# Kernel tuning notes

Measured on AMD Instinct MI355X. Metric: run time of the kernel, lower is better.

## Reference

```python
import jax, jax.numpy as jnp
import numpy as np

S = 3      # num_scales
CIN = 3    # in_channels (hardcoded by expand(...,3,...) in source)
COUT = 3   # out_channels (forced by final broadcast)
K = 3
PAD = 1


def setup_inputs() -> dict:
    key = jax.random.key(0)
    ks = jax.random.split(key, 8)
    B, H, W = 4, 384, 384
    x = jax.random.normal(ks[0], (B, CIN, H, W), jnp.float32)
    # params follow the torch inits: theta,sigma ~ U(0,pi); f0,theta0 = 1
    theta = jax.random.uniform(ks[1], (S, COUT, CIN), jnp.float32) * jnp.pi
    sigma = jax.random.uniform(ks[2], (S, COUT, CIN), jnp.float32) * jnp.pi
    f0 = jnp.ones((S, COUT, CIN), jnp.float32)
    theta0 = jnp.ones((S, COUT, CIN), jnp.float32)
    attn_w1 = jax.random.normal(ks[3], (64, CIN), jnp.float32) * 0.1     # 1x1 conv weight
    attn_b1 = jnp.zeros((64,), jnp.float32)
    attn_w2 = jax.random.normal(ks[4], (COUT * S, 64), jnp.float32) * 0.1
    attn_b2 = jnp.zeros((COUT * S,), jnp.float32)
    conv_w = jax.random.normal(ks[5], (COUT, CIN, K, K), jnp.float32) * 0.05
    mixing = jax.random.uniform(ks[6], (1,), jnp.float32)
    band = jax.random.uniform(ks[7], (COUT, CIN, 2), jnp.float32)        # freq_band_select ~ U(0,1)
    return dict(x=x, theta=theta, sigma=sigma, f0=f0, theta0=theta0,
                attn_w1=attn_w1, attn_b1=attn_b1, attn_w2=attn_w2, attn_b2=attn_b2,
                conv_w=conv_w, mixing=mixing, band=band)


def _log_gabor_bank(theta, sigma, f0, theta0, H, W):
    # vectorized over all scales: returns [S, Co, Cin, H, W] real filter bank
    yy, xx = jnp.meshgrid(jnp.linspace(-1.0, 1.0, H), jnp.linspace(-1.0, 1.0, W), indexing='ij')
    r = jnp.sqrt(xx * xx + yy * yy + 1e-6)          # [H,W]
    phi = jnp.arctan2(yy, xx)                        # [H,W]
    f0e = f0[..., None, None]                        # [S,Co,Cin,1,1]
    sig = sigma[..., None, None]
    th = theta[..., None, None]
    th0 = theta0[..., None, None]
    log_gabor = jnp.exp(-jnp.log(r - jnp.log(f0e)) ** 2 / (2.0 * jnp.log(sig) ** 2))
    angular = jnp.exp(-(phi - th) ** 2 / (2.0 * th0 ** 2))
    return log_gabor * angular


def _forward(x, theta, sigma, f0, theta0, attn_w1, attn_b1, attn_w2, attn_b2, conv_w, mixing, band):
    B, Cin, H, W = x.shape
    # torch.fft.fftshift with no dim shifts ALL axes (incl. batch/channel) -- replicate exactly
    x_freq_shift = jnp.fft.fftshift(jnp.fft.fft2(x))                 # [B,Cin,H,W] complex64

    filt = _log_gabor_bank(theta, sigma, f0, theta0, H, W)           # [S,Co,Cin,H,W]

    # attention net: 1x1 conv -> relu -> 1x1 conv -> softmax over channel dim
    mag = jnp.abs(x_freq_shift)
    h1 = jax.nn.relu(jnp.einsum('bchw,oc->bohw', mag, attn_w1) + attn_b1[None, :, None, None])
    logits = jnp.einsum('bchw,oc->bohw', h1, attn_w2) + attn_b2[None, :, None, None]
    attn = jax.nn.softmax(logits, axis=1).reshape(B, S, COUT, H, W)

    # attended[b,d,h,w] = sum_{s,co} attn[b,s,co,h,w] * xfreq[b,d,h,w] * filt[s,co,d,h,w]
    wgt = jnp.einsum('bschw,scdhw->bdhw', attn, filt)                # real [B,Cin,H,W]
    attended = (x_freq_shift * wgt).sum(axis=1)                      # [B,H,W] complex

    # per-(out,in)-channel square band mask, indices from height (as in source)
    start_idx = jnp.floor((band[..., 0] + 1.0) / 2.0 * H).astype(jnp.int32)   # [Co,Cin]
    end_idx = jnp.floor((band[..., 1] + 1.0) / 2.0 * H).astype(jnp.int32)
    ih = jnp.arange(H)
    rm = (ih[None, None, :] >= start_idx[..., None]) & (ih[None, None, :] < end_idx[..., None])
    iw = jnp.arange(W)
    cm = (iw[None, None, :] >= start_idx[..., None]) & (iw[None, None, :] < end_idx[..., None])
    mask = (rm[..., :, None] & cm[..., None, :]).astype(x.dtype)     # [Co,Cin,H,W]

    # broadcast quirk in source: [B,1,H,W] * [B,Co,1,Cin,H,W] -> [B,Co,B,Cin,H,W]
    six = mask[None, :, None, :, :, :] * attended[None, None, :, None, :, :]
    six = jnp.broadcast_to(six, (B, COUT, B, Cin, H, W))
    # torch ifftshift with no dim shifts ALL 6 axes; ifft2 transforms last two
    x_filtered = jnp.fft.ifft2(jnp.fft.ifftshift(six)).real          # [B,Co,B,Cin,H,W]

    x_spatial = jax.lax.conv_general_dilated(
        x, conv_w, window_strides=(1, 1), padding=[(PAD, PAD), (PAD, PAD)],
        dimension_numbers=('NCHW', 'OIHW', 'NCHW'))                  # [B,Co,H,W]

    mix = mixing[0]
    return mix * x_filtered + (1.0 - mix) * x_spatial[None, None]    # [B,Co,B,Cin,H,W]


def reference(x, theta, sigma, f0, theta0, attn_w1, attn_b1, attn_w2, attn_b2, conv_w, mixing, band):
    return _forward(x, theta, sigma, f0, theta0, attn_w1, attn_b1, attn_w2, attn_b2, conv_w, mixing, band)
```

## Files before the change

kernel.cpp:

```cpp
#include <hip/hip_runtime.h>
#include <math.h>

#define N384 384
#define NPIX 147456
#define LSTRIDE 385
#define LINES 8

__device__ __forceinline__ float2 cmul(float2 a, float2 b) {
    return make_float2(a.x*b.x - a.y*b.y, a.x*b.y + a.y*b.x);
}

__device__ __forceinline__ void build_tw(float2* tw, int tid) {
    for (int k = tid; k < 384; k += 256) {
        float sn, cs;
        sincospif((float)k * (2.0f / 384.0f), &sn, &cs);
        tw[k] = make_float2(cs, sn);
    }
}

template <int SGNI>
__device__ float2* fft384x8(float2* b0, float2* b1, const float2* tw, int tid) {
    float2* src = b0;
    float2* dst = b1;
    const int line = tid >> 5;
    const int l32  = tid & 31;
    const float SG = (float)SGNI;

    {
        const float s3 = SG * 0.86602540378443864676f;
        float2* L = src + line * LSTRIDE;
        float2* D = dst + line * LSTRIDE;
#pragma unroll
        for (int q = 0; q < 4; ++q) {
            int j = l32 + 32 * q;
            float2 a0 = L[j], a1 = L[j + 128], a2 = L[j + 256];
            float t1x = a1.x + a2.x, t1y = a1.y + a2.y;
            float t2x = a1.x - a2.x, t2y = a1.y - a2.y;
            float2 bb0 = make_float2(a0.x + t1x, a0.y + t1y);
            float mx = a0.x - 0.5f * t1x, my = a0.y - 0.5f * t1y;
            float ux = -s3 * t2y, uy = s3 * t2x;
            float2 bb1 = make_float2(mx + ux, my + uy);
            float2 bb2 = make_float2(mx - ux, my - uy);
            float2 t  = tw[j];
            float2 t2 = tw[2 * j];
            float2 w  = make_float2(t.x,  SG * t.y);
            float2 w2 = make_float2(t2.x, SG * t2.y);
            D[3 * j]     = bb0;
            D[3 * j + 1] = cmul(bb1, w);
            D[3 * j + 2] = cmul(bb2, w2);
        }
    }
    __syncthreads();
    { float2* t = src; src = dst; dst = t; }

#pragma unroll
    for (int st = 0; st < 3; ++st) {
        const int s = 3 << (2 * st);
        float2* L = src + line * LSTRIDE;
        float2* D = dst + line * LSTRIDE;
#pragma unroll
        for (int q = 0; q < 3; ++q) {
            int i = l32 + 32 * q;
            int k = i % s;
            int js = i - k;
            float2 A0 = L[i];
            float2 A1 = L[i + 96];
            float2 A2 = L[i + 192];
            float2 A3 = L[i + 288];
            float t0x = A0.x + A2.x, t0y = A0.y + A2.y;
            float t1x = A0.x - A2.x, t1y = A0.y - A2.y;
            float t2x = A1.x + A3.x, t2y = A1.y + A3.y;
            float t3x = A1.x - A3.x, t3y = A1.y - A3.y;
            float u3x = -SG * t3y,   u3y = SG * t3x;
            float2 y0 = make_float2(t0x + t2x, t0y + t2y);
            float2 y2 = make_float2(t0x - t2x, t0y - t2y);
            float2 y1 = make_float2(t1x + u3x, t1y + u3y);
            float2 y3 = make_float2(t1x - u3x, t1y - u3y);
            float2 c1 = tw[js], c2 = tw[2 * js], c3 = tw[3 * js];
            float2 w1 = make_float2(c1.x, SG * c1.y);
            float2 w2 = make_float2(c2.x, SG * c2.y);
            float2 w3 = make_float2(c3.x, SG * c3.y);
            int o = i + 3 * js;
            D[o]         = y0;
            D[o + s]     = cmul(y1, w1);
            D[o + 2 * s] = cmul(y2, w2);
            D[o + 3 * s] = cmul(y3, w3);
        }
        __syncthreads();
        { float2* t = src; src = dst; dst = t; }
    }

    {
        float2* L = src + line * LSTRIDE;
        float2* D = dst + line * LSTRIDE;
#pragma unroll
        for (int q = 0; q < 6; ++q) {
            int i = l32 + 32 * q;
            float2 a = L[i], b = L[i + 192];
            D[i]       = make_float2(a.x + b.x, a.y + b.y);
            D[i + 192] = make_float2(a.x - b.x, a.y - b.y);
        }
    }
    __syncthreads();
    return dst;
}

__global__ __launch_bounds__(256) void k_fwd_rows(const float* __restrict__ x,
                                                  float2* __restrict__ F1) {
    __shared__ float2 sbuf[2][LINES * LSTRIDE];
    __shared__ float2 tw[384];
    int img = blockIdx.y;
    int rg  = blockIdx.x;
    int tid = threadIdx.x;
    build_tw(tw, tid);
    const float4* xim = (const float4*)(x + (size_t)img * NPIX + (size_t)rg * 16 * 384);
    for (int idx4 = tid; idx4 < 1536; idx4 += 256) {
        int row = idx4 / 96;
        int e   = (idx4 - row * 96) * 4;
        float4 v = xim[idx4];
        float* L = (float*)(sbuf[0] + (row >> 1) * LSTRIDE + e) + (row & 1);
        L[0] = v.x; L[2] = v.y; L[4] = v.z; L[6] = v.w;
    }
    __syncthreads();
    float2* res = fft384x8<-1>(sbuf[0], sbuf[1], tw, tid);
    float2* F1b = F1 + (size_t)img * NPIX + (size_t)rg * 16 * 384;
    for (int it = tid; it < 1536; it += 256) {
        int line = it / 192;
        int k2   = it - line * 192;
        const float2* L = res + line * LSTRIDE;
        float2 A = L[k2];
        int m = (k2 == 0) ? 0 : 384 - k2;
        float2 B = L[m];
        float2 X1 = make_float2(0.5f * (A.x + B.x), 0.5f * (A.y - B.y));
        float2 X2 = make_float2(0.5f * (A.y + B.y), 0.5f * (B.x - A.x));
        F1b[(size_t)(2 * line) * 384 + k2]     = X1;
        F1b[(size_t)(2 * line + 1) * 384 + k2] = X2;
    }
}

__global__ __launch_bounds__(256) void k_fwd_cols(const float2* __restrict__ In,
                                                  float2* __restrict__ Out) {
    __shared__ float2 sbuf[2][LINES * LSTRIDE];
    __shared__ float2 tw[384];
    int img = blockIdx.y;
    int cg  = blockIdx.x;
    int tid = threadIdx.x;
    build_tw(tw, tid);
    const float4* inim = (const float4*)(In + (size_t)img * NPIX + cg * 8);
    int c = tid & 3, hb = tid >> 2;
    for (int q = 0; q < 6; ++q) {
        int h = hb + 64 * q;
        float4 v = inim[(size_t)h * 192 + c];
        sbuf[0][(2 * c) * LSTRIDE + h]     = make_float2(v.x, v.y);
        sbuf[0][(2 * c + 1) * LSTRIDE + h] = make_float2(v.z, v.w);
    }
    __syncthreads();
    float2* res = fft384x8<-1>(sbuf[0], sbuf[1], tw, tid);
    float4* outim = (float4*)(Out + (size_t)img * NPIX + cg * 8);
    for (int q = 0; q < 3; ++q) {
        int h = hb + 64 * q;
        float2 a = res[(2 * c) * LSTRIDE + h];
        float2 b = res[(2 * c + 1) * LSTRIDE + h];
        outim[(size_t)h * 192 + c] = make_float4(a.x, a.y, b.x, b.y);
    }
}

__global__ __launch_bounds__(192) void k_attn(const float2* __restrict__ F2,
                                              const float* __restrict__ theta,
                                              const float* __restrict__ sigma,
                                              const float* __restrict__ f0,
                                              const float* __restrict__ theta0,
                                              const float* __restrict__ aw1,
                                              const float* __restrict__ ab1,
                                              const float* __restrict__ aw2,
                                              const float* __restrict__ ab2,
                                              const float* __restrict__ band,
                                              float2* __restrict__ A) {
    __shared__ float4 par[27];
    int tid = threadIdx.x;
    if (tid < 27) {
        float lf0 = logf(f0[tid]);
        float ls  = logf(sigma[tid]);
        float na  = -0.5f / (ls * ls);
        float th  = theta[tid];
        float t0  = theta0[tid];
        float nb  = -0.5f / (t0 * t0);
        par[tid] = make_float4(lf0, na, th, nb);
    }
    __syncthreads();

    int h = 192 + blockIdx.x;
    int w = 192 + tid;

    bool needed = false;
#pragma unroll
    for (int q = 0; q < 9; ++q) {
        int s = (int)floorf((band[2 * q + 0] + 1.0f) * 0.5f * 384.0f);
        int e = (int)floorf((band[2 * q + 1] + 1.0f) * 0.5f * 384.0f);
        needed |= (h >= s) && (h < e) && (w >= s) && (w < e);
    }
    if (__ballot(needed) == 0ULL) return;

    int hs = h - 192;
    int ws = w - 192;

    float2 xf[4][3];
    float  mag[4][3];
#pragma unroll
    for (int b = 0; b < 4; ++b) {
        int bp = (b + 2) & 3;
#pragma unroll
        for (int c = 0; c < 3; ++c) {
            int cp = c + 2; if (cp >= 3) cp -= 3;
            float2 v = F2[(size_t)(bp * 3 + cp) * NPIX + (size_t)hs * 384 + ws];
            xf[b][c]  = v;
            mag[b][c] = sqrtf(v.x * v.x + v.y * v.y);
        }
    }

    float lgt[4][9];
#pragma unroll
    for (int b = 0; b < 4; ++b)
#pragma unroll
        for (int j = 0; j < 9; ++j) lgt[b][j] = ab2[j];
    for (int o = 0; o < 64; ++o) {
        float w0 = aw1[o * 3 + 0], w1 = aw1[o * 3 + 1], w2 = aw1[o * 3 + 2];
        float bb = ab1[o];
        float hv[4];
#pragma unroll
        for (int b = 0; b < 4; ++b)
            hv[b] = fmaxf(bb + w0 * mag[b][0] + w1 * mag[b][1] + w2 * mag[b][2], 0.0f);
#pragma unroll
        for (int j = 0; j < 9; ++j) {
            float wj = aw2[j * 64 + o];
#pragma unroll
            for (int b = 0; b < 4; ++b) lgt[b][j] += wj * hv[b];
        }
    }

    float yy = -1.0f + 2.0f * (float)h / 383.0f;
    float xx = -1.0f + 2.0f * (float)w / 383.0f;
    float r   = sqrtf(xx * xx + yy * yy + 1e-6f);
    float phi = atan2f(yy, xx);
    float filt[27];
#pragma unroll
    for (int i = 0; i < 27; ++i) {
        float4 pr = par[i];
        float lr = logf(r - pr.x);
        float dphi = phi - pr.z;
        filt[i] = expf(lr * lr * pr.y + dphi * dphi * pr.w);
    }

#pragma unroll
    for (int b = 0; b < 4; ++b) {
        float mxv = lgt[b][0];
#pragma unroll
        for (int j = 1; j < 9; ++j) mxv = fmaxf(mxv, lgt[b][j]);
        float e[9];
        float se = 0.0f;
#pragma unroll
        for (int j = 0; j < 9; ++j) { e[j] = expf(lgt[b][j] - mxv); se += e[j]; }
        float inv = 1.0f / se;

        float2 acc = make_float2(0.0f, 0.0f);
#pragma unroll
        for (int d = 0; d < 3; ++d) {
            float wg = 0.0f;
#pragma unroll
            for (int s = 0; s < 3; ++s)
#pragma unroll
                for (int co = 0; co < 3; ++co)
                    wg += e[s * 3 + co] * filt[(s * 3 + co) * 3 + d];
            wg *= inv;
            acc.x += xf[b][d].x * wg;
            acc.y += xf[b][d].y * wg;
        }
        if (needed)
            A[(size_t)b * NPIX + (size_t)h * 384 + w] = acc;
    }
}

__global__ __launch_bounds__(256) void k_conv(const float* __restrict__ x,
                                              const float* __restrict__ cw,
                                              float* __restrict__ xsp) {
    int p = blockIdx.x * 256 + threadIdx.x;
    int w = p % 384;
    int t = p / 384;
    int h = t % 384; t /= 384;
    int o = t % 3;
    int b = t / 3;
    float acc = 0.0f;
    const float* xb = x + (size_t)b * 3 * NPIX;
#pragma unroll
    for (int ci = 0; ci < 3; ++ci) {
        const float* xc = xb + (size_t)ci * NPIX;
#pragma unroll
        for (int kh = 0; kh < 3; ++kh) {
            int hh = h + kh - 1;
            if (hh < 0 || hh >= 384) continue;
#pragma unroll
            for (int kw = 0; kw < 3; ++kw) {
                int ww = w + kw - 1;
                if (ww < 0 || ww >= 384) continue;
                acc += xc[(size_t)hh * 384 + ww] * cw[((o * 3 + ci) * 3 + kh) * 3 + kw];
            }
        }
    }
    xsp[p] = acc;
}

__global__ __launch_bounds__(256) void k_masked_rows(const float2* __restrict__ A,
                                                     const float* __restrict__ band,
                                                     float2* __restrict__ G1c) {
    int ii  = blockIdx.y;
    int rg  = blockIdx.x;
    int cop = ii / 12;
    int bp  = (ii / 3) % 4;
    int dp  = ii % 3;
    int pidx = (cop * 3 + dp) * 2;
    int sidx = (int)floorf((band[pidx + 0] + 1.0f) * 0.5f * 384.0f);
    int eidx = (int)floorf((band[pidx + 1] + 1.0f) * 0.5f * 384.0f);
    if (eidx <= sidx) return;
    int h0 = 192 + rg * 8;
    if (h0 + 8 <= sidx || h0 >= eidx) return;

    __shared__ float2 sbuf[2][LINES * LSTRIDE];
    __shared__ float2 tw[384];
    int tid = threadIdx.x;
    build_tw(tw, tid);
    const float2* Ab = A + (size_t)bp * NPIX;
    for (int idx = tid; idx < 8 * 384; idx += 256) {
        int line = idx / 384;
        int w    = idx - line * 384;
        int h    = h0 + line;
        bool m = (h >= sidx) && (h < eidx) && (w >= sidx) && (w < eidx);
        float2 v = make_float2(0.0f, 0.0f);
        if (m) v = Ab[(size_t)h * 384 + w];
        sbuf[0][line * LSTRIDE + w] = v;
    }
    __syncthreads();
    float2* res = fft384x8<1>(sbuf[0], sbuf[1], tw, tid);
    for (int idx = tid; idx < 8 * 384; idx += 256) {
        int line = idx / 384;
        int w    = idx - line * 384;
        int h    = h0 + line;
        if (h >= sidx && h < eidx) {
            float2 v = res[line * LSTRIDE + w];
            if (w & 1) { v.x = -v.x; v.y = -v.y; }
            G1c[((size_t)ii * 192 + (h - sidx)) * 384 + w] = v;
        }
    }
}

__global__ __launch_bounds__(256) void k_col_gemm_combine(const float2* __restrict__ G1c,
                                                          const float* __restrict__ band,
                                                          const float* __restrict__ xsp,
                                                          const float* __restrict__ mixing,
                                                          float* __restrict__ out) {
    __shared__ float2 tw[384];
    int tid = threadIdx.x;
    build_tw(tw, tid);

    int ii  = blockIdx.y;
    int gt  = blockIdx.x * 256 + tid;
    int wq  = gt % 96;
    int hg  = gt / 96;
    int w   = wq * 4;
    int h0  = hg * 4;

    int cop = ii / 12;
    int bp  = (ii / 3) % 4;
    int dp  = ii % 3;
    int pidx = (cop * 3 + dp) * 2;
    int sidx = (int)floorf((band[pidx + 0] + 1.0f) * 0.5f * 384.0f);
    int eidx = (int)floorf((band[pidx + 1] + 1.0f) * 0.5f * 384.0f);
    __syncthreads();

    float acc[4][4];
#pragma unroll
    for (int kh = 0; kh < 4; ++kh)
#pragma unroll
        for (int j = 0; j < 4; ++j) acc[kh][j] = 0.0f;

    int idx0 = (sidx * (h0 + 0)) % 384;
    int idx1 = (sidx * (h0 + 1)) % 384;
    int idx2 = (sidx * (h0 + 2)) % 384;
    int idx3 = (sidx * (h0 + 3)) % 384;
    const int s0 = h0, s1 = h0 + 1, s2 = h0 + 2, s3 = h0 + 3;

    const float4* g = (const float4*)(G1c + (size_t)ii * 192 * 384 + w);
    for (int hp = sidx; hp < eidx; ++hp) {
        float4 g0 = g[(size_t)(hp - sidx) * 192];
        float4 g1 = g[(size_t)(hp - sidx) * 192 + 1];
        float2 t0 = tw[idx0];
        float2 t1 = tw[idx1];
        float2 t2 = tw[idx2];
        float2 t3 = tw[idx3];
        acc[0][0] += t0.x * g0.x - t0.y * g0.y;
        acc[0][1] += t0.x * g0.z - t0.y * g0.w;
        acc[0][2] += t0.x * g1.x - t0.y * g1.y;
        acc[0][3] += t0.x * g1.z - t0.y * g1.w;
        acc[1][0] += t1.x * g0.x - t1.y * g0.y;
        acc[1][1] += t1.x * g0.z - t1.y * g0.w;
        acc[1][2] += t1.x * g1.x - t1.y * g1.y;
        acc[1][3] += t1.x * g1.z - t1.y * g1.w;
        acc[2][0] += t2.x * g0.x - t2.y * g0.y;
        acc[2][1] += t2.x * g0.z - t2.y * g0.w;
        acc[2][2] += t2.x * g1.x - t2.y * g1.y;
        acc[2][3] += t2.x * g1.z - t2.y * g1.w;
        acc[3][0] += t3.x * g0.x - t3.y * g0.y;
        acc[3][1] += t3.x * g0.z - t3.y * g0.w;
        acc[3][2] += t3.x * g1.x - t3.y * g1.y;
        acc[3][3] += t3.x * g1.z - t3.y * g1.w;
        idx0 += s0; if (idx0 >= 384) idx0 -= 384;
        idx1 += s1; if (idx1 >= 384) idx1 -= 384;
        idx2 += s2; if (idx2 >= 384) idx2 -= 384;
        idx3 += s3; if (idx3 >= 384) idx3 -= 384;
    }

    int co = cop + 2; if (co >= 3) co -= 3;
    int b  = (bp + 2) & 3;
    int d  = dp + 2;  if (d >= 3) d -= 3;
    float mix  = mixing[0];
    float omix = 1.0f - mix;
    const float invn2 = 1.0f / 147456.0f;
    const float* xs = xsp + (size_t)(b * 3 + d) * NPIX;
    float* obase = out + (size_t)(co * 12 + b * 3 + d) * NPIX;
#pragma unroll
    for (int kh = 0; kh < 4; ++kh) {
        int h = h0 + kh;
        float sgn = (h & 1) ? -invn2 : invn2;
        size_t off = (size_t)h * 384 + w;
        float4 xv = *(const float4*)(xs + off);
        float4 val;
        val.x = mix * (acc[kh][0] * sgn) + omix * xv.x;
        val.y = mix * (acc[kh][1] * sgn) + omix * xv.y;
        val.z = mix * (acc[kh][2] * sgn) + omix * xv.z;
        val.w = mix * (acc[kh][3] * sgn) + omix * xv.w;
#pragma unroll
        for (int a = 0; a < 4; ++a)
            *(float4*)(obase + off + (size_t)a * 5308416) = val;
    }
}

extern "C" void kernel_launch(void* const* d_in, const int* in_sizes, int n_in,
                              void* d_out, int out_size, void* d_ws, size_t ws_size,
                              hipStream_t stream) {
    const float* x      = (const float*)d_in[0];
    const float* theta  = (const float*)d_in[1];
    const float* sigma  = (const float*)d_in[2];
    const float* f0     = (const float*)d_in[3];
    const float* theta0 = (const float*)d_in[4];
    const float* aw1    = (const float*)d_in[5];
    const float* ab1    = (const float*)d_in[6];
    const float* aw2    = (const float*)d_in[7];
    const float* ab2    = (const float*)d_in[8];
    const float* cw     = (const float*)d_in[9];
    const float* mixing = (const float*)d_in[10];
    const float* band   = (const float*)d_in[11];
    float* out = (float*)d_out;

    float2* F1  = (float2*)d_ws;
    float2* F2  = F1 + (size_t)12 * NPIX;
    float2* G1c = (float2*)d_ws;
    float2* A   = (float2*)d_ws + (size_t)36 * NPIX;
    float*  xsp = (float*)((float2*)d_ws + (size_t)40 * NPIX);

    k_fwd_rows<<<dim3(24, 12), 256, 0, stream>>>(x, F1);
    k_fwd_cols<<<dim3(24, 12), 256, 0, stream>>>(F1, F2);
    k_attn<<<192, 192, 0, stream>>>(F2, theta, sigma, f0, theta0,
                                    aw1, ab1, aw2, ab2, band, A);
    k_conv<<<6912, 256, 0, stream>>>(x, cw, xsp);
    k_masked_rows<<<dim3(24, 36), 256, 0, stream>>>(A, band, G1c);
    k_col_gemm_combine<<<dim3(36, 36), 256, 0, stream>>>(G1c, band, xsp, mixing, out);
}
```

Before: 208.4 us.

## Fuse 3x3 spatial conv into combine kernel and use radix-6 FFT stages

Removes the separate conv kernel and its xsp buffer; each combine thread now computes its 4x4 conv outputs directly from x with a 6x6 register window. This drops one launch and the global write and re-read of the conv result, but conv work is repeated for each of the 36 combine slices, where before it was computed once. The shared 384-point FFT is also refactored from radix 3·4·4·4·2 into radix 6·4·4·4, cutting one stage and one __syncthreads.

```diff
diff --git a/kernel.cpp b/kernel.cpp
--- a/kernel.cpp
+++ b/kernel.cpp
@@ -25,37 +25,54 @@
     const int line = tid >> 5;
     const int l32  = tid & 31;
     const float SG = (float)SGNI;
+    const float s3 = SG * 0.86602540378443864676f;
 
     {
-        const float s3 = SG * 0.86602540378443864676f;
         float2* L = src + line * LSTRIDE;
         float2* D = dst + line * LSTRIDE;
 #pragma unroll
-        for (int q = 0; q < 4; ++q) {
-            int j = l32 + 32 * q;
-            float2 a0 = L[j], a1 = L[j + 128], a2 = L[j + 256];
-            float t1x = a1.x + a2.x, t1y = a1.y + a2.y;
-            float t2x = a1.x - a2.x, t2y = a1.y - a2.y;
-            float2 bb0 = make_float2(a0.x + t1x, a0.y + t1y);
-            float mx = a0.x - 0.5f * t1x, my = a0.y - 0.5f * t1y;
+        for (int q = 0; q < 2; ++q) {
+            int i = l32 + 32 * q;
+            float2 e0 = L[i],       e1 = L[i + 128], e2 = L[i + 256];
+            float2 o0 = L[i + 64],  o1 = L[i + 192], o2 = L[i + 320];
+            float t1x = e1.x + e2.x, t1y = e1.y + e2.y;
+            float t2x = e1.x - e2.x, t2y = e1.y - e2.y;
+            float2 E0 = make_float2(e0.x + t1x, e0.y + t1y);
+            float mx = e0.x - 0.5f * t1x, my = e0.y - 0.5f * t1y;
             float ux = -s3 * t2y, uy = s3 * t2x;
-            float2 bb1 = make_float2(mx + ux, my + uy);
-            float2 bb2 = make_float2(mx - ux, my - uy);
-            float2 t  = tw[j];
-            float2 t2 = tw[2 * j];
-            float2 w  = make_float2(t.x,  SG * t.y);
-            float2 w2 = make_float2(t2.x, SG * t2.y);
-            D[3 * j]     = bb0;
-            D[3 * j + 1] = cmul(bb1, w);
-            D[3 * j + 2] = cmul(bb2, w2);
+            float2 E1 = make_float2(mx + ux, my + uy);
+            float2 E2 = make_float2(mx - ux, my - uy);
+            float s1x = o1.x + o2.x, s1y = o1.y + o2.y;
+            float s2x = o1.x - o2.x, s2y = o1.y - o2.y;
+            float2 O0 = make_float2(o0.x + s1x, o0.y + s1y);
+            float nx = o0.x - 0.5f * s1x, ny = o0.y - 0.5f * s1y;
+            float vx = -s3 * s2y, vy = s3 * s2x;
+            float2 O1 = make_float2(nx + vx, ny + vy);
+            float2 O2 = make_float2(nx - vx, ny - vy);
+            float2 T1 = make_float2(0.5f * O1.x - s3 * O1.y, 0.5f * O1.y + s3 * O1.x);
+            float2 T2 = make_float2(-0.5f * O2.x - s3 * O2.y, -0.5f * O2.y + s3 * O2.x);
+            float2 y0 = make_float2(E0.x + O0.x, E0.y + O0.y);
+            float2 y3 = make_float2(E0.x - O0.x, E0.y - O0.y);
+            float2 y1 = make_float2(E1.x + T1.x, E1.y + T1.y);
+            float2 y4 = make_float2(E1.x - T1.x, E1.y - T1.y);
+            float2 y2 = make_float2(E2.x + T2.x, E2.y + T2.y);
+            float2 y5 = make_float2(E2.x - T2.x, E2.y - T2.y);
+            float2 c1 = tw[i], c2 = tw[2 * i], c3 = tw[3 * i], c4 = tw[4 * i], c5 = tw[5 * i];
+            int o = 6 * i;
+            D[o]     = y0;
+            D[o + 1] = cmul(y1, make_float2(c1.x, SG * c1.y));
+            D[o + 2] = cmul(y2, make_float2(c2.x, SG * c2.y));
+            D[o + 3] = cmul(y3, make_float2(c3.x, SG * c3.y));
+            D[o + 4] = cmul(y4, make_float2(c4.x, SG * c4.y));
+            D[o + 5] = cmul(y5, make_float2(c5.x, SG * c5.y));
         }
     }
     __syncthreads();
     { float2* t = src; src = dst; dst = t; }
 
 #pragma unroll
-    for (int st = 0; st < 3; ++st) {
-        const int s = 3 << (2 * st);
+    for (int st = 0; st < 2; ++st) {
+        const int s = (st == 0) ? 6 : 24;
         float2* L = src + line * LSTRIDE;
         float2* D = dst + line * LSTRIDE;
 #pragma unroll
@@ -94,11 +111,21 @@
         float2* L = src + line * LSTRIDE;
         float2* D = dst + line * LSTRIDE;
 #pragma unroll
-        for (int q = 0; q < 6; ++q) {
+        for (int q = 0; q < 3; ++q) {
             int i = l32 + 32 * q;
-            float2 a = L[i], b = L[i + 192];
-            D[i]       = make_float2(a.x + b.x, a.y + b.y);
-            D[i + 192] = make_float2(a.x - b.x, a.y - b.y);
+            float2 A0 = L[i];
+            float2 A1 = L[i + 96];
+            float2 A2 = L[i + 192];
+            float2 A3 = L[i + 288];
+            float t0x = A0.x + A2.x, t0y = A0.y + A2.y;
+            float t1x = A0.x - A2.x, t1y = A0.y - A2.y;
+            float t2x = A1.x + A3.x, t2y = A1.y + A3.y;
+            float t3x = A1.x - A3.x, t3y = A1.y - A3.y;
+            float u3x = -SG * t3y,   u3y = SG * t3x;
+            D[i]       = make_float2(t0x + t2x, t0y + t2y);
+            D[i + 96]  = make_float2(t1x + u3x, t1y + u3y);
+            D[i + 192] = make_float2(t0x - t2x, t0y - t2y);
+            D[i + 288] = make_float2(t1x - u3x, t1y - u3y);
         }
     }
     __syncthreads();
@@ -280,35 +307,6 @@
     }
 }
 
-__global__ __launch_bounds__(256) void k_conv(const float* __restrict__ x,
-                                              const float* __restrict__ cw,
-                                              float* __restrict__ xsp) {
-    int p = blockIdx.x * 256 + threadIdx.x;
-    int w = p % 384;
-    int t = p / 384;
-    int h = t % 384; t /= 384;
-    int o = t % 3;
-    int b = t / 3;
-    float acc = 0.0f;
-    const float* xb = x + (size_t)b * 3 * NPIX;
-#pragma unroll
-    for (int ci = 0; ci < 3; ++ci) {
-        const float* xc = xb + (size_t)ci * NPIX;
-#pragma unroll
-        for (int kh = 0; kh < 3; ++kh) {
-            int hh = h + kh - 1;
-            if (hh < 0 || hh >= 384) continue;
-#pragma unroll
-            for (int kw = 0; kw < 3; ++kw) {
-                int ww = w + kw - 1;
-                if (ww < 0 || ww >= 384) continue;
-                acc += xc[(size_t)hh * 384 + ww] * cw[((o * 3 + ci) * 3 + kh) * 3 + kw];
-            }
-        }
-    }
-    xsp[p] = acc;
-}
-
 __global__ __launch_bounds__(256) void k_masked_rows(const float2* __restrict__ A,
                                                      const float* __restrict__ band,
                                                      float2* __restrict__ G1c) {
@@ -354,7 +352,8 @@
 
 __global__ __launch_bounds__(256) void k_col_gemm_combine(const float2* __restrict__ G1c,
                                                           const float* __restrict__ band,
-                                                          const float* __restrict__ xsp,
+                                                          const float* __restrict__ x,
+                                                          const float* __restrict__ cw,
                                                           const float* __restrict__ mixing,
                                                           float* __restrict__ out) {
     __shared__ float2 tw[384];
@@ -421,22 +420,57 @@
     int co = cop + 2; if (co >= 3) co -= 3;
     int b  = (bp + 2) & 3;
     int d  = dp + 2;  if (d >= 3) d -= 3;
+
+    float cacc[4][4];
+#pragma unroll
+    for (int kh = 0; kh < 4; ++kh)
+#pragma unroll
+        for (int j = 0; j < 4; ++j) cacc[kh][j] = 0.0f;
+    const float* xb = x + (size_t)b * 3 * NPIX;
+#pragma unroll
+    for (int ci = 0; ci < 3; ++ci) {
+        const float* xc = xb + (size_t)ci * NPIX;
+        const float* w9 = cw + ((size_t)d * 3 + ci) * 9;
+        float wv[9];
+#pragma unroll
+        for (int t = 0; t < 9; ++t) wv[t] = w9[t];
+#pragma unroll
+        for (int ihh = 0; ihh < 6; ++ihh) {
+            int hh = h0 - 1 + ihh;
+            if (hh < 0 || hh >= 384) continue;
+            float v[6];
+#pragma unroll
+            for (int c6 = 0; c6 < 6; ++c6) {
+                int ww = w - 1 + c6;
+                v[c6] = (ww >= 0 && ww < 384) ? xc[(size_t)hh * 384 + ww] : 0.0f;
+            }
+#pragma unroll
+            for (int kh = 0; kh < 4; ++kh) {
+                int r = ihh - kh;
+                if (r < 0 || r > 2) continue;
+#pragma unroll
+                for (int j = 0; j < 4; ++j)
+#pragma unroll
+                    for (int kw = 0; kw < 3; ++kw)
+                        cacc[kh][j] += v[j + kw] * wv[r * 3 + kw];
+            }
+        }
+    }
+
     float mix  = mixing[0];
     float omix = 1.0f - mix;
     const float invn2 = 1.0f / 147456.0f;
-    const float* xs = xsp + (size_t)(b * 3 + d) * NPIX;
     float* obase = out + (size_t)(co * 12 + b * 3 + d) * NPIX;
 #pragma unroll
     for (int kh = 0; kh < 4; ++kh) {
         int h = h0 + kh;
         float sgn = (h & 1) ? -invn2 : invn2;
         size_t off = (size_t)h * 384 + w;
-        float4 xv = *(const float4*)(xs + off);
         float4 val;
-        val.x = mix * (acc[kh][0] * sgn) + omix * xv.x;
-        val.y = mix * (acc[kh][1] * sgn) + omix * xv.y;
-        val.z = mix * (acc[kh][2] * sgn) + omix * xv.z;
-        val.w = mix * (acc[kh][3] * sgn) + omix * xv.w;
+        val.x = mix * (acc[kh][0] * sgn) + omix * cacc[kh][0];
+        val.y = mix * (acc[kh][1] * sgn) + omix * cacc[kh][1];
+        val.z = mix * (acc[kh][2] * sgn) + omix * cacc[kh][2];
+        val.w = mix * (acc[kh][3] * sgn) + omix * cacc[kh][3];
 #pragma unroll
         for (int a = 0; a < 4; ++a)
             *(float4*)(obase + off + (size_t)a * 5308416) = val;
@@ -464,13 +498,11 @@
     float2* F2  = F1 + (size_t)12 * NPIX;
     float2* G1c = (float2*)d_ws;
     float2* A   = (float2*)d_ws + (size_t)36 * NPIX;
-    float*  xsp = (float*)((float2*)d_ws + (size_t)40 * NPIX);
 
     k_fwd_rows<<<dim3(24, 12), 256, 0, stream>>>(x, F1);
     k_fwd_cols<<<dim3(24, 12), 256, 0, stream>>>(F1, F2);
     k_attn<<<192, 192, 0, stream>>>(F2, theta, sigma, f0, theta0,
                                     aw1, ab1, aw2, ab2, band, A);
-    k_conv<<<6912, 256, 0, stream>>>(x, cw, xsp);
     k_masked_rows<<<dim3(24, 36), 256, 0, stream>>>(A, band, G1c);
-    k_col_gemm_combine<<<dim3(36, 36), 256, 0, stream>>>(G1c, band, xsp, mixing, out);
-}
+    k_col_gemm_combine<<<dim3(36, 36), 256, 0, stream>>>(G1c, band, x, cw, mixing, out);
+}
```

Result: no change. 205.0 us (-1.6%).
